# Kernel optimization log

Measured on AMD Instinct MI355X. Metric: run time of the kernel, lower is better.

## Reference

```python
import jax, jax.numpy as jnp
import numpy as np

N_NODES = 50000
N_EDGES = 800000
H = 128
LN_EPS = 1e-5


def setup_inputs() -> dict:
    key = jax.random.key(0)
    ks = jax.random.split(key, 8)
    x = jax.random.normal(ks[0], (N_NODES, H), dtype=jnp.float32)
    edge_index = jax.random.randint(ks[1], (2, N_EDGES), 0, N_NODES, dtype=jnp.int64)
    # edge_attention MLP params: Linear(2H -> H), ReLU, Linear(H -> 1), Sigmoid
    W1 = jax.random.normal(ks[2], (2 * H, H), dtype=jnp.float32) * 0.02
    b1 = jnp.zeros((H,), dtype=jnp.float32)
    W2 = jax.random.normal(ks[3], (H, 1), dtype=jnp.float32) * 0.02
    b2 = jnp.zeros((1,), dtype=jnp.float32)
    # LayerNorm affine params
    gamma = jnp.ones((H,), dtype=jnp.float32)
    beta = jnp.zeros((H,), dtype=jnp.float32)
    return {"x": x, "edge_index": edge_index, "W1": W1, "b1": b1,
            "W2": W2, "b2": b2, "gamma": gamma, "beta": beta}


def reference(x, edge_index, W1, b1, W2, b2, gamma, beta):
    src = edge_index[0]
    tgt = edge_index[1]
    # per-edge gated weight: sigmoid(MLP([x_src, x_tgt]))  -> [E]
    edge_feat = jnp.concatenate([x[src], x[tgt]], axis=1)        # [E, 2H]
    h = jax.nn.relu(edge_feat @ W1 + b1)                          # [E, H]
    w = jax.nn.sigmoid(h @ W2 + b2)[:, 0]                         # [E]
    # scatter-add weighted source features into targets (fused replacement
    # for the per-node Python loop in the original)
    agg = jax.ops.segment_sum(w[:, None] * x[src], tgt,
                              num_segments=x.shape[0])            # [N, H]
    attended = x + agg
    # LayerNorm over last dim
    mu = jnp.mean(attended, axis=-1, keepdims=True)
    var = jnp.mean(jnp.square(attended - mu), axis=-1, keepdims=True)
    out = (attended - mu) * jax.lax.rsqrt(var + LN_EPS) * gamma + beta
    return out
```

## Files before the change

kernel.cpp:

```cpp
#include <hip/hip_runtime.h>

static __device__ __forceinline__ unsigned short f2bf(float f) {
    union { float f; unsigned int u; } c; c.f = f;
    unsigned int u = c.u;
    return (unsigned short)((u + 0x7FFFu + ((u >> 16) & 1u)) >> 16);
}
static __device__ __forceinline__ float bflo(unsigned int uu) {
    union { unsigned int u; float f; } c; c.u = uu << 16; return c.f;
}
static __device__ __forceinline__ float bfhi(unsigned int uu) {
    union { unsigned int u; float f; } c; c.u = uu & 0xffff0000u; return c.f;
}
static __device__ __forceinline__ unsigned char f2fp8(float f) {
    int enc = __builtin_amdgcn_cvt_pk_fp8_f32(f, f, 0, false);
    return (unsigned char)(enc & 0xff);
}

typedef __bf16 bf16x8 __attribute__((ext_vector_type(8)));
typedef float  f32x4  __attribute__((ext_vector_type(4)));
typedef float  f32x2  __attribute__((ext_vector_type(2)));

__global__ void k_pack(const float* __restrict__ W1, unsigned short* __restrict__ Bt,
                       int* __restrict__ rowstart, int N) {
    int idx = blockIdx.x * blockDim.x + threadIdx.x;
    if (idx < 256 * 128) {
        int j = idx >> 7, k = idx & 127;
        int r = (j < 128) ? k : (128 + k);
        int c = j & 127;
        Bt[idx] = f2bf(W1[r * 128 + c]);
    }
    if (idx <= N) rowstart[idx] = 0;
}

__global__ __launch_bounds__(256) void k_gemm(const float* __restrict__ x,
                                              const unsigned short* __restrict__ Bt,
                                              const float* __restrict__ b1,
                                              unsigned char* __restrict__ U,
                                              unsigned short* __restrict__ V,
                                              unsigned short* __restrict__ XB, int M) {
    int wave = threadIdx.x >> 6, lane = threadIdx.x & 63;
    int row0 = blockIdx.x * 64 + wave * 16;
    int col0 = blockIdx.y * 64;
    int lr = lane & 15;
    int lk = (lane >> 4) << 3;

    f32x4 acc[4] = {};
    int arow = row0 + lr;
    bool in = (arow < M);
    const float* xr = x + (size_t)arow * 128;
    bool emit_xb = (blockIdx.y == 0);

#pragma unroll
    for (int kk = 0; kk < 4; ++kk) {
        int k = kk * 32 + lk;
        union { bf16x8 v; unsigned short u[8]; } ua;
        if (in) {
            float4 f0 = *(const float4*)(xr + k);
            float4 f1 = *(const float4*)(xr + k + 4);
            ua.u[0] = f2bf(f0.x); ua.u[1] = f2bf(f0.y);
            ua.u[2] = f2bf(f0.z); ua.u[3] = f2bf(f0.w);
            ua.u[4] = f2bf(f1.x); ua.u[5] = f2bf(f1.y);
            ua.u[6] = f2bf(f1.z); ua.u[7] = f2bf(f1.w);
        } else {
#pragma unroll
            for (int i = 0; i < 8; ++i) ua.u[i] = 0;
        }
        if (emit_xb && in) *(bf16x8*)(XB + (size_t)arow * 128 + k) = ua.v;
#pragma unroll
        for (int nf = 0; nf < 4; ++nf) {
            int col = col0 + nf * 16 + lr;
            bf16x8 b = *(const bf16x8*)(Bt + col * 128 + k);
            acc[nf] = __builtin_amdgcn_mfma_f32_16x16x32_bf16(ua.v, b, acc[nf], 0, 0, 0);
        }
    }
    int rb = row0 + ((lane >> 4) << 2);
    if (col0 < 128) {
#pragma unroll
        for (int nf = 0; nf < 4; ++nf) {
            int feat = col0 + nf * 16 + lr;
#pragma unroll
            for (int r = 0; r < 4; ++r) {
                int node = rb + r;
                if (node < M) U[(size_t)node * 128 + feat] = f2fp8(acc[nf][r]);
            }
        }
    } else {
#pragma unroll
        for (int nf = 0; nf < 4; ++nf) {
            int feat = col0 + nf * 16 + lr - 128;
            float bias = b1[feat];
#pragma unroll
            for (int r = 0; r < 4; ++r) {
                int node = rb + r;
                if (node < M) V[(size_t)node * 128 + feat] = f2bf(acc[nf][r] + bias);
            }
        }
    }
}

__global__ void k_hist(const int* __restrict__ ei, int* __restrict__ deg,
                       int* __restrict__ rank, int E) {
    int e = blockIdx.x * blockDim.x + threadIdx.x;
    if (e < E) rank[e] = atomicAdd(deg + ei[E + e], 1);
}

__global__ void k_scan1(int* __restrict__ a, int* __restrict__ bsum, int N) {
    __shared__ int s0[256], s1[256];
    int tid = threadIdx.x;
    int n = blockIdx.x * 256 + tid;
    int v = (n < N) ? a[n] : 0;
    s0[tid] = v;
    __syncthreads();
    int* cur = s0; int* nxt = s1;
#pragma unroll
    for (int off = 1; off < 256; off <<= 1) {
        int val = cur[tid];
        if (tid >= off) val += cur[tid - off];
        nxt[tid] = val;
        __syncthreads();
        int* t = cur; cur = nxt; nxt = t;
    }
    if (n < N) a[n] = cur[tid] - v;
    if (tid == 255) bsum[blockIdx.x] = cur[255];
}

__global__ void k_scan2(int* __restrict__ bsum, int nb) {
    __shared__ int s0[256], s1[256];
    int tid = threadIdx.x;
    int v = (tid < nb) ? bsum[tid] : 0;
    s0[tid] = v;
    __syncthreads();
    int* cur = s0; int* nxt = s1;
#pragma unroll
    for (int off = 1; off < 256; off <<= 1) {
        int val = cur[tid];
        if (tid >= off) val += cur[tid - off];
        nxt[tid] = val;
        __syncthreads();
        int* t = cur; cur = nxt; nxt = t;
    }
    if (tid < nb) bsum[tid] = cur[tid] - v;
}

__global__ void k_scan3(int* __restrict__ rowstart, const int* __restrict__ bsum,
                        int N, int E) {
    int n = blockIdx.x * 256 + threadIdx.x;
    if (n < N) rowstart[n] = rowstart[n] + bsum[n >> 8];
    if (n == 0) rowstart[N] = E;
}

__global__ void k_scatter(const int* __restrict__ ei, const int* __restrict__ rowstart,
                          const int* __restrict__ rank, int* __restrict__ esrc, int E) {
    int e = blockIdx.x * blockDim.x + threadIdx.x;
    if (e < E) {
        int s = ei[e];
        int t = ei[E + e];
        esrc[rowstart[t] + rank[e]] = s;
    }
}

template <int USE_XB>
__global__ __launch_bounds__(256) void k_fused(const float* __restrict__ x,
                                               const unsigned char* __restrict__ U,
                                               const unsigned short* __restrict__ V,
                                               const unsigned short* __restrict__ XB,
                                               const int* __restrict__ rowstart,
                                               const int* __restrict__ esrc,
                                               const float* __restrict__ W2,
                                               const float* __restrict__ b2,
                                               const float* __restrict__ gamma,
                                               const float* __restrict__ beta,
                                               float* __restrict__ out, int N) {
    int row = blockIdx.x * 4 + (threadIdx.x >> 6);
    if (row >= N) return;
    int lane = threadIdx.x & 63;
    int el = lane & 7;
    int q  = lane >> 3;

    float w2r[16];
#pragma unroll
    for (int i = 0; i < 16; ++i) w2r[i] = W2[16 * q + i];
    float b2s = b2[0];

    const unsigned short* vp = V + (size_t)row * 128 + 16 * q;
    uint4 va = *(const uint4*)vp;
    uint4 vb = *(const uint4*)(vp + 8);
    float vf[16];
    vf[0]  = bflo(va.x); vf[1]  = bfhi(va.x);
    vf[2]  = bflo(va.y); vf[3]  = bfhi(va.y);
    vf[4]  = bflo(va.z); vf[5]  = bfhi(va.z);
    vf[6]  = bflo(va.w); vf[7]  = bfhi(va.w);
    vf[8]  = bflo(vb.x); vf[9]  = bfhi(vb.x);
    vf[10] = bflo(vb.y); vf[11] = bfhi(vb.y);
    vf[12] = bflo(vb.z); vf[13] = bfhi(vb.z);
    vf[14] = bflo(vb.w); vf[15] = bfhi(vb.w);

    int st = rowstart[row];
    int en = rowstart[row + 1];

    float2 xx = *(const float2*)(x + (size_t)row * 128 + 2 * lane);
    float a0 = xx.x, a1 = xx.y;

    for (int g = st; g < en; g += 8) {
        int e = g + el;
        bool val = (e < en);
        int s = val ? esrc[e] : 0;

        uint4 ua = *(const uint4*)(U + (size_t)s * 128 + 16 * q);
        f32x2 d0 = __builtin_amdgcn_cvt_pk_f32_fp8(ua.x, false);
        f32x2 d1 = __builtin_amdgcn_cvt_pk_f32_fp8(ua.x, true);
        f32x2 d2 = __builtin_amdgcn_cvt_pk_f32_fp8(ua.y, false);
        f32x2 d3 = __builtin_amdgcn_cvt_pk_f32_fp8(ua.y, true);
        f32x2 d4 = __builtin_amdgcn_cvt_pk_f32_fp8(ua.z, false);
        f32x2 d5 = __builtin_amdgcn_cvt_pk_f32_fp8(ua.z, true);
        f32x2 d6 = __builtin_amdgcn_cvt_pk_f32_fp8(ua.w, false);
        f32x2 d7 = __builtin_amdgcn_cvt_pk_f32_fp8(ua.w, true);

        float p = 0.0f;
        p = fmaf(fmaxf(d0.x + vf[0],  0.f), w2r[0],  p);
        p = fmaf(fmaxf(d0.y + vf[1],  0.f), w2r[1],  p);
        p = fmaf(fmaxf(d1.x + vf[2],  0.f), w2r[2],  p);
        p = fmaf(fmaxf(d1.y + vf[3],  0.f), w2r[3],  p);
        p = fmaf(fmaxf(d2.x + vf[4],  0.f), w2r[4],  p);
        p = fmaf(fmaxf(d2.y + vf[5],  0.f), w2r[5],  p);
        p = fmaf(fmaxf(d3.x + vf[6],  0.f), w2r[6],  p);
        p = fmaf(fmaxf(d3.y + vf[7],  0.f), w2r[7],  p);
        p = fmaf(fmaxf(d4.x + vf[8],  0.f), w2r[8],  p);
        p = fmaf(fmaxf(d4.y + vf[9],  0.f), w2r[9],  p);
        p = fmaf(fmaxf(d5.x + vf[10], 0.f), w2r[10], p);
        p = fmaf(fmaxf(d5.y + vf[11], 0.f), w2r[11], p);
        p = fmaf(fmaxf(d6.x + vf[12], 0.f), w2r[12], p);
        p = fmaf(fmaxf(d6.y + vf[13], 0.f), w2r[13], p);
        p = fmaf(fmaxf(d7.x + vf[14], 0.f), w2r[14], p);
        p = fmaf(fmaxf(d7.y + vf[15], 0.f), w2r[15], p);

        p += __shfl_xor(p, 8);
        p += __shfl_xor(p, 16);
        p += __shfl_xor(p, 32);

        float w = val ? 1.0f / (1.0f + __expf(-(p + b2s))) : 0.0f;

#pragma unroll
        for (int j = 0; j < 8; ++j) {
            float wj = __shfl(w, j);
            int   sj = __shfl(s, j);
            if (USE_XB) {
                unsigned int xv = *(const unsigned int*)(XB + (size_t)sj * 128 + 2 * lane);
                a0 = fmaf(wj, bflo(xv), a0);
                a1 = fmaf(wj, bfhi(xv), a1);
            } else {
                float2 xf = *(const float2*)(x + (size_t)sj * 128 + 2 * lane);
                a0 = fmaf(wj, xf.x, a0);
                a1 = fmaf(wj, xf.y, a1);
            }
        }
    }

    float s = a0 + a1;
#pragma unroll
    for (int off = 32; off; off >>= 1) s += __shfl_xor(s, off);
    float mu = s * (1.0f / 128.0f);
    float d0v = a0 - mu, d1v = a1 - mu;
    float qq = d0v * d0v + d1v * d1v;
#pragma unroll
    for (int off = 32; off; off >>= 1) qq += __shfl_xor(qq, off);
    float rstd = rsqrtf(qq * (1.0f / 128.0f) + 1e-5f);
    float2 gg = *(const float2*)(gamma + 2 * lane);
    float2 bb = *(const float2*)(beta + 2 * lane);
    float2 o;
    o.x = d0v * rstd * gg.x + bb.x;
    o.y = d1v * rstd * gg.y + bb.y;
    *(float2*)(out + (size_t)row * 128 + 2 * lane) = o;
}

extern "C" void kernel_launch(void* const* d_in, const int* in_sizes, int n_in,
                              void* d_out, int out_size, void* d_ws, size_t ws_size,
                              hipStream_t stream) {
    const float* x     = (const float*)d_in[0];
    const int*   ei    = (const int*)d_in[1];
    const float* W1    = (const float*)d_in[2];
    const float* b1    = (const float*)d_in[3];
    const float* W2    = (const float*)d_in[4];
    const float* b2    = (const float*)d_in[5];
    const float* gamma = (const float*)d_in[6];
    const float* beta  = (const float*)d_in[7];
    float* out = (float*)d_out;

    const int N = in_sizes[0] / 128;
    const int E = in_sizes[1] / 2;
    const int NB = (N + 255) / 256;

    char* w = (char*)d_ws;
    size_t off = 0;
    auto alloc = [&](size_t bytes) {
        char* p = w + off;
        off = (off + bytes + 255) & ~(size_t)255;
        return p;
    };
    unsigned short* Bt       = (unsigned short*)alloc(256 * 128 * 2);
    unsigned char*  U        = (unsigned char*)alloc((size_t)N * 128);
    unsigned short* V        = (unsigned short*)alloc((size_t)N * 128 * 2);
    int*            rowstart = (int*)alloc((size_t)(N + 1) * 4);
    int*            bsum     = (int*)alloc(256 * 4);
    int*            rank     = (int*)alloc((size_t)E * 4);
    int*            esrc     = (int*)alloc((size_t)E * 4);
    size_t off_noxb = off;
    unsigned short* XB       = (unsigned short*)alloc((size_t)N * 128 * 2);
    bool use_xb = (off <= ws_size);
    if (!use_xb) { XB = nullptr; off = off_noxb; }

    int PB = (N + 256) / 256;
    if (PB < 128) PB = 128;
    k_pack<<<PB, 256, 0, stream>>>(W1, Bt, rowstart, N);

    dim3 ggrid((N + 63) / 64, 4);
    k_gemm<<<ggrid, 256, 0, stream>>>(x, Bt, b1, U, V, XB, N);

    k_hist<<<(E + 255) / 256, 256, 0, stream>>>(ei, rowstart, rank, E);

    k_scan1<<<NB, 256, 0, stream>>>(rowstart, bsum, N);
    k_scan2<<<1, 256, 0, stream>>>(bsum, NB);
    k_scan3<<<NB, 256, 0, stream>>>(rowstart, bsum, N, E);

    k_scatter<<<(E + 255) / 256, 256, 0, stream>>>(ei, rowstart, rank, esrc, E);

    if (use_xb)
        k_fused<1><<<(N + 3) / 4, 256, 0, stream>>>(x, U, V, XB, rowstart, esrc,
                                                    W2, b2, gamma, beta, out, N);
    else
        k_fused<0><<<(N + 3) / 4, 256, 0, stream>>>(x, U, V, XB, rowstart, esrc,
                                                    W2, b2, gamma, beta, out, N);
}
```

Baseline: 171.3 us.

## Fuse weight packing with degree histogram, widen GEMM tiles, read bf16 self features

Merges the W1 packing kernel with the edge-degree histogram kernel and replaces the rowstart zeroing with a memset, removing one launch. The GEMM now computes 128 output columns per block across a 2-wide grid instead of 64 columns across 4, so each block converts its x rows once for twice the MFMA work. The fused aggregation kernel reads the node's own features from the bf16 copy instead of fp32 x, halving that load at some precision cost in the residual. The wider tile raises register use per thread and may lower occupancy.

Result: slower. 177.5 us (+3.6%).

```diff
diff --git a/kernel.cpp b/kernel.cpp
--- a/kernel.cpp
+++ b/kernel.cpp
@@ -20,8 +20,9 @@
 typedef float  f32x4  __attribute__((ext_vector_type(4)));
 typedef float  f32x2  __attribute__((ext_vector_type(2)));
 
-__global__ void k_pack(const float* __restrict__ W1, unsigned short* __restrict__ Bt,
-                       int* __restrict__ rowstart, int N) {
+__global__ void k_packhist(const float* __restrict__ W1, unsigned short* __restrict__ Bt,
+                           const int* __restrict__ ei, int* __restrict__ deg,
+                           int* __restrict__ rank, int E) {
     int idx = blockIdx.x * blockDim.x + threadIdx.x;
     if (idx < 256 * 128) {
         int j = idx >> 7, k = idx & 127;
@@ -29,7 +30,9 @@
         int c = j & 127;
         Bt[idx] = f2bf(W1[r * 128 + c]);
     }
-    if (idx <= N) rowstart[idx] = 0;
+    int nthreads = gridDim.x * blockDim.x;
+    for (int e = idx; e < E; e += nthreads)
+        rank[e] = atomicAdd(deg + ei[E + e], 1);
 }
 
 __global__ __launch_bounds__(256) void k_gemm(const float* __restrict__ x,
@@ -40,15 +43,18 @@
                                               unsigned short* __restrict__ XB, int M) {
     int wave = threadIdx.x >> 6, lane = threadIdx.x & 63;
     int row0 = blockIdx.x * 64 + wave * 16;
-    int col0 = blockIdx.y * 64;
+    int col0 = blockIdx.y * 128;
     int lr = lane & 15;
     int lk = (lane >> 4) << 3;
 
-    f32x4 acc[4] = {};
+    f32x4 acc[8];
+#pragma unroll
+    for (int i = 0; i < 8; ++i) acc[i] = (f32x4){0.f, 0.f, 0.f, 0.f};
+
     int arow = row0 + lr;
     bool in = (arow < M);
     const float* xr = x + (size_t)arow * 128;
-    bool emit_xb = (blockIdx.y == 0);
+    bool emit_xb = (XB != nullptr) && (blockIdx.y == 0);
 
 #pragma unroll
     for (int kk = 0; kk < 4; ++kk) {
@@ -67,17 +73,17 @@
         }
         if (emit_xb && in) *(bf16x8*)(XB + (size_t)arow * 128 + k) = ua.v;
 #pragma unroll
-        for (int nf = 0; nf < 4; ++nf) {
+        for (int nf = 0; nf < 8; ++nf) {
             int col = col0 + nf * 16 + lr;
             bf16x8 b = *(const bf16x8*)(Bt + col * 128 + k);
             acc[nf] = __builtin_amdgcn_mfma_f32_16x16x32_bf16(ua.v, b, acc[nf], 0, 0, 0);
         }
     }
     int rb = row0 + ((lane >> 4) << 2);
-    if (col0 < 128) {
-#pragma unroll
-        for (int nf = 0; nf < 4; ++nf) {
-            int feat = col0 + nf * 16 + lr;
+    if (blockIdx.y == 0) {
+#pragma unroll
+        for (int nf = 0; nf < 8; ++nf) {
+            int feat = nf * 16 + lr;
 #pragma unroll
             for (int r = 0; r < 4; ++r) {
                 int node = rb + r;
@@ -86,8 +92,8 @@
         }
     } else {
 #pragma unroll
-        for (int nf = 0; nf < 4; ++nf) {
-            int feat = col0 + nf * 16 + lr - 128;
+        for (int nf = 0; nf < 8; ++nf) {
+            int feat = nf * 16 + lr;
             float bias = b1[feat];
 #pragma unroll
             for (int r = 0; r < 4; ++r) {
@@ -96,12 +102,6 @@
             }
         }
     }
-}
-
-__global__ void k_hist(const int* __restrict__ ei, int* __restrict__ deg,
-                       int* __restrict__ rank, int E) {
-    int e = blockIdx.x * blockDim.x + threadIdx.x;
-    if (e < E) rank[e] = atomicAdd(deg + ei[E + e], 1);
 }
 
 __global__ void k_scan1(int* __restrict__ a, int* __restrict__ bsum, int N) {
@@ -198,8 +198,14 @@
     int st = rowstart[row];
     int en = rowstart[row + 1];
 
-    float2 xx = *(const float2*)(x + (size_t)row * 128 + 2 * lane);
-    float a0 = xx.x, a1 = xx.y;
+    float a0, a1;
+    if (USE_XB) {
+        unsigned int xv = *(const unsigned int*)(XB + (size_t)row * 128 + 2 * lane);
+        a0 = bflo(xv); a1 = bfhi(xv);
+    } else {
+        float2 xx = *(const float2*)(x + (size_t)row * 128 + 2 * lane);
+        a0 = xx.x; a1 = xx.y;
+    }
 
     for (int g = st; g < en; g += 8) {
         int e = g + el;
@@ -309,14 +315,12 @@
     bool use_xb = (off <= ws_size);
     if (!use_xb) { XB = nullptr; off = off_noxb; }
 
-    int PB = (N + 256) / 256;
-    if (PB < 128) PB = 128;
-    k_pack<<<PB, 256, 0, stream>>>(W1, Bt, rowstart, N);
-
-    dim3 ggrid((N + 63) / 64, 4);
+    hipMemsetAsync(rowstart, 0, (size_t)(N + 1) * 4, stream);
+
+    k_packhist<<<(E + 255) / 256, 256, 0, stream>>>(W1, Bt, ei, rowstart, rank, E);
+
+    dim3 ggrid((N + 63) / 64, 2);
     k_gemm<<<ggrid, 256, 0, stream>>>(x, Bt, b1, U, V, XB, N);
-
-    k_hist<<<(E + 255) / 256, 256, 0, stream>>>(ei, rowstart, rank, E);
 
     k_scan1<<<NB, 256, 0, stream>>>(rowstart, bsum, N);
     k_scan2<<<1, 256, 0, stream>>>(bsum, NB);
```

## Unroll edge loop by two, merge scan passes, read self row from bf16

Applied to the files above, without the earlier changes.

The fused aggregation loop now handles 16 edges per iteration as two independent groups of 8. This doubles the gathers and shuffles in flight to hide the latency of the random loads. The second and third scan kernels are merged into one, where each block rescans the block sums itself, removing one launch. The node's own row is now read from the bf16 copy, which slightly changes precision for the residual term, and the gemm skips writing XB when it is null.

New measurement: 174.5 us. No clear change (+1.9%).

```diff
diff --git a/kernel.cpp b/kernel.cpp
--- a/kernel.cpp
+++ b/kernel.cpp
@@ -19,6 +19,36 @@
 typedef __bf16 bf16x8 __attribute__((ext_vector_type(8)));
 typedef float  f32x4  __attribute__((ext_vector_type(4)));
 typedef float  f32x2  __attribute__((ext_vector_type(2)));
+
+static __device__ __forceinline__ float mlp16(uint4 ua, const float* __restrict__ vf,
+                                              const float* __restrict__ w2r) {
+    f32x2 d0 = __builtin_amdgcn_cvt_pk_f32_fp8(ua.x, false);
+    f32x2 d1 = __builtin_amdgcn_cvt_pk_f32_fp8(ua.x, true);
+    f32x2 d2 = __builtin_amdgcn_cvt_pk_f32_fp8(ua.y, false);
+    f32x2 d3 = __builtin_amdgcn_cvt_pk_f32_fp8(ua.y, true);
+    f32x2 d4 = __builtin_amdgcn_cvt_pk_f32_fp8(ua.z, false);
+    f32x2 d5 = __builtin_amdgcn_cvt_pk_f32_fp8(ua.z, true);
+    f32x2 d6 = __builtin_amdgcn_cvt_pk_f32_fp8(ua.w, false);
+    f32x2 d7 = __builtin_amdgcn_cvt_pk_f32_fp8(ua.w, true);
+    float p = 0.0f;
+    p = fmaf(fmaxf(d0.x + vf[0],  0.f), w2r[0],  p);
+    p = fmaf(fmaxf(d0.y + vf[1],  0.f), w2r[1],  p);
+    p = fmaf(fmaxf(d1.x + vf[2],  0.f), w2r[2],  p);
+    p = fmaf(fmaxf(d1.y + vf[3],  0.f), w2r[3],  p);
+    p = fmaf(fmaxf(d2.x + vf[4],  0.f), w2r[4],  p);
+    p = fmaf(fmaxf(d2.y + vf[5],  0.f), w2r[5],  p);
+    p = fmaf(fmaxf(d3.x + vf[6],  0.f), w2r[6],  p);
+    p = fmaf(fmaxf(d3.y + vf[7],  0.f), w2r[7],  p);
+    p = fmaf(fmaxf(d4.x + vf[8],  0.f), w2r[8],  p);
+    p = fmaf(fmaxf(d4.y + vf[9],  0.f), w2r[9],  p);
+    p = fmaf(fmaxf(d5.x + vf[10], 0.f), w2r[10], p);
+    p = fmaf(fmaxf(d5.y + vf[11], 0.f), w2r[11], p);
+    p = fmaf(fmaxf(d6.x + vf[12], 0.f), w2r[12], p);
+    p = fmaf(fmaxf(d6.y + vf[13], 0.f), w2r[13], p);
+    p = fmaf(fmaxf(d7.x + vf[14], 0.f), w2r[14], p);
+    p = fmaf(fmaxf(d7.y + vf[15], 0.f), w2r[15], p);
+    return p;
+}
 
 __global__ void k_pack(const float* __restrict__ W1, unsigned short* __restrict__ Bt,
                        int* __restrict__ rowstart, int N) {
@@ -48,7 +78,7 @@
     int arow = row0 + lr;
     bool in = (arow < M);
     const float* xr = x + (size_t)arow * 128;
-    bool emit_xb = (blockIdx.y == 0);
+    bool emit_xb = (XB != nullptr) && (blockIdx.y == 0);
 
 #pragma unroll
     for (int kk = 0; kk < 4; ++kk) {
@@ -124,11 +154,11 @@
     if (tid == 255) bsum[blockIdx.x] = cur[255];
 }
 
-__global__ void k_scan2(int* __restrict__ bsum, int nb) {
+__global__ void k_scan23(int* __restrict__ rowstart, const int* __restrict__ bsum,
+                         int nb, int N, int E) {
     __shared__ int s0[256], s1[256];
     int tid = threadIdx.x;
-    int v = (tid < nb) ? bsum[tid] : 0;
-    s0[tid] = v;
+    s0[tid] = (tid < nb) ? bsum[tid] : 0;
     __syncthreads();
     int* cur = s0; int* nxt = s1;
 #pragma unroll
@@ -139,13 +169,10 @@
         __syncthreads();
         int* t = cur; cur = nxt; nxt = t;
     }
-    if (tid < nb) bsum[tid] = cur[tid] - v;
-}
-
-__global__ void k_scan3(int* __restrict__ rowstart, const int* __restrict__ bsum,
-                        int N, int E) {
-    int n = blockIdx.x * 256 + threadIdx.x;
-    if (n < N) rowstart[n] = rowstart[n] + bsum[n >> 8];
+    int b = blockIdx.x;
+    int offset = (b == 0) ? 0 : cur[b - 1];
+    int n = b * 256 + tid;
+    if (n < N) rowstart[n] += offset;
     if (n == 0) rowstart[N] = E;
 }
 
@@ -198,60 +225,56 @@
     int st = rowstart[row];
     int en = rowstart[row + 1];
 
-    float2 xx = *(const float2*)(x + (size_t)row * 128 + 2 * lane);
-    float a0 = xx.x, a1 = xx.y;
-
-    for (int g = st; g < en; g += 8) {
-        int e = g + el;
-        bool val = (e < en);
-        int s = val ? esrc[e] : 0;
-
-        uint4 ua = *(const uint4*)(U + (size_t)s * 128 + 16 * q);
-        f32x2 d0 = __builtin_amdgcn_cvt_pk_f32_fp8(ua.x, false);
-        f32x2 d1 = __builtin_amdgcn_cvt_pk_f32_fp8(ua.x, true);
-        f32x2 d2 = __builtin_amdgcn_cvt_pk_f32_fp8(ua.y, false);
-        f32x2 d3 = __builtin_amdgcn_cvt_pk_f32_fp8(ua.y, true);
-        f32x2 d4 = __builtin_amdgcn_cvt_pk_f32_fp8(ua.z, false);
-        f32x2 d5 = __builtin_amdgcn_cvt_pk_f32_fp8(ua.z, true);
-        f32x2 d6 = __builtin_amdgcn_cvt_pk_f32_fp8(ua.w, false);
-        f32x2 d7 = __builtin_amdgcn_cvt_pk_f32_fp8(ua.w, true);
-
-        float p = 0.0f;
-        p = fmaf(fmaxf(d0.x + vf[0],  0.f), w2r[0],  p);
-        p = fmaf(fmaxf(d0.y + vf[1],  0.f), w2r[1],  p);
-        p = fmaf(fmaxf(d1.x + vf[2],  0.f), w2r[2],  p);
-        p = fmaf(fmaxf(d1.y + vf[3],  0.f), w2r[3],  p);
-        p = fmaf(fmaxf(d2.x + vf[4],  0.f), w2r[4],  p);
-        p = fmaf(fmaxf(d2.y + vf[5],  0.f), w2r[5],  p);
-        p = fmaf(fmaxf(d3.x + vf[6],  0.f), w2r[6],  p);
-        p = fmaf(fmaxf(d3.y + vf[7],  0.f), w2r[7],  p);
-        p = fmaf(fmaxf(d4.x + vf[8],  0.f), w2r[8],  p);
-        p = fmaf(fmaxf(d4.y + vf[9],  0.f), w2r[9],  p);
-        p = fmaf(fmaxf(d5.x + vf[10], 0.f), w2r[10], p);
-        p = fmaf(fmaxf(d5.y + vf[11], 0.f), w2r[11], p);
-        p = fmaf(fmaxf(d6.x + vf[12], 0.f), w2r[12], p);
-        p = fmaf(fmaxf(d6.y + vf[13], 0.f), w2r[13], p);
-        p = fmaf(fmaxf(d7.x + vf[14], 0.f), w2r[14], p);
-        p = fmaf(fmaxf(d7.y + vf[15], 0.f), w2r[15], p);
-
-        p += __shfl_xor(p, 8);
-        p += __shfl_xor(p, 16);
-        p += __shfl_xor(p, 32);
-
-        float w = val ? 1.0f / (1.0f + __expf(-(p + b2s))) : 0.0f;
+    float a0, a1;
+    if (USE_XB) {
+        unsigned int xv = *(const unsigned int*)(XB + (size_t)row * 128 + 2 * lane);
+        a0 = bflo(xv); a1 = bfhi(xv);
+    } else {
+        float2 xx = *(const float2*)(x + (size_t)row * 128 + 2 * lane);
+        a0 = xx.x; a1 = xx.y;
+    }
+
+    for (int g = st; g < en; g += 16) {
+        int e0 = g + el;
+        int e1 = g + 8 + el;
+        bool v0 = (e0 < en);
+        bool v1 = (e1 < en);
+        int s0 = v0 ? esrc[e0] : 0;
+        int s1 = v1 ? esrc[e1] : 0;
+
+        uint4 ua0 = *(const uint4*)(U + (size_t)s0 * 128 + 16 * q);
+        uint4 ua1 = *(const uint4*)(U + (size_t)s1 * 128 + 16 * q);
+
+        float p0 = mlp16(ua0, vf, w2r);
+        float p1 = mlp16(ua1, vf, w2r);
+
+        p0 += __shfl_xor(p0, 8);  p1 += __shfl_xor(p1, 8);
+        p0 += __shfl_xor(p0, 16); p1 += __shfl_xor(p1, 16);
+        p0 += __shfl_xor(p0, 32); p1 += __shfl_xor(p1, 32);
+
+        float w0 = v0 ? 1.0f / (1.0f + __expf(-(p0 + b2s))) : 0.0f;
+        float w1 = v1 ? 1.0f / (1.0f + __expf(-(p1 + b2s))) : 0.0f;
 
 #pragma unroll
         for (int j = 0; j < 8; ++j) {
-            float wj = __shfl(w, j);
-            int   sj = __shfl(s, j);
+            int   sj0 = __shfl(s0, j);
+            int   sj1 = __shfl(s1, j);
+            float wj0 = __shfl(w0, j);
+            float wj1 = __shfl(w1, j);
             if (USE_XB) {
-                unsigned int xv = *(const unsigned int*)(XB + (size_t)sj * 128 + 2 * lane);
-                a0 = fmaf(wj, bflo(xv), a0);
-                a1 = fmaf(wj, bfhi(xv), a1);
+                unsigned int xv0 = *(const unsigned int*)(XB + (size_t)sj0 * 128 + 2 * lane);
+                unsigned int xv1 = *(const unsigned int*)(XB + (size_t)sj1 * 128 + 2 * lane);
+                a0 = fmaf(wj0, bflo(xv0), a0);
+                a1 = fmaf(wj0, bfhi(xv0), a1);
+                a0 = fmaf(wj1, bflo(xv1), a0);
+                a1 = fmaf(wj1, bfhi(xv1), a1);
             } else {
-                float2 xf = *(const float2*)(x + (size_t)sj * 128 + 2 * lane);
-                a0 = fmaf(wj, xf.x, a0);
-                a1 = fmaf(wj, xf.y, a1);
+                float2 xf0 = *(const float2*)(x + (size_t)sj0 * 128 + 2 * lane);
+                float2 xf1 = *(const float2*)(x + (size_t)sj1 * 128 + 2 * lane);
+                a0 = fmaf(wj0, xf0.x, a0);
+                a1 = fmaf(wj0, xf0.y, a1);
+                a0 = fmaf(wj1, xf1.x, a0);
+                a1 = fmaf(wj1, xf1.y, a1);
             }
         }
     }
@@ -319,8 +342,7 @@
     k_hist<<<(E + 255) / 256, 256, 0, stream>>>(ei, rowstart, rank, E);
 
     k_scan1<<<NB, 256, 0, stream>>>(rowstart, bsum, N);
-    k_scan2<<<1, 256, 0, stream>>>(bsum, NB);
-    k_scan3<<<NB, 256, 0, stream>>>(rowstart, bsum, N, E);
+    k_scan23<<<NB, 256, 0, stream>>>(rowstart, bsum, NB, N, E);
 
     k_scatter<<<(E + 255) / 256, 256, 0, stream>>>(ei, rowstart, rank, esrc, E);
 
```

## Fuse prep kernels, merge scan passes, and read bf16 x everywhere

Applied to the files above, without the earlier changes.

Weight packing, the x-to-bf16 conversion and the degree histogram are merged into one grid-stride prep kernel, and the rowstart zeroing moves to a memset. The GEMM now reads the precomputed bf16 XB instead of converting fp32 x itself. Scan passes 2 and 3 are merged, with each block redundantly scanning the block sums. The fused kernel now takes the residual x from bf16 XB, which lowers precision, and the fp32 fallback for a small workspace is removed.

Result: no change. 171.2 us (-0.0%).

```diff
diff --git a/kernel.cpp b/kernel.cpp
--- a/kernel.cpp
+++ b/kernel.cpp
@@ -20,24 +20,35 @@
 typedef float  f32x4  __attribute__((ext_vector_type(4)));
 typedef float  f32x2  __attribute__((ext_vector_type(2)));
 
-__global__ void k_pack(const float* __restrict__ W1, unsigned short* __restrict__ Bt,
-                       int* __restrict__ rowstart, int N) {
+__global__ void k_prep(const float* __restrict__ W1, unsigned short* __restrict__ Bt,
+                       const float* __restrict__ x, unsigned short* __restrict__ XB,
+                       const int* __restrict__ ei, int* __restrict__ deg,
+                       int* __restrict__ rank, int NH4 , int E) {
     int idx = blockIdx.x * blockDim.x + threadIdx.x;
+    int T = gridDim.x * blockDim.x;
+
     if (idx < 256 * 128) {
         int j = idx >> 7, k = idx & 127;
         int r = (j < 128) ? k : (128 + k);
-        int c = j & 127;
-        Bt[idx] = f2bf(W1[r * 128 + c]);
-    }
-    if (idx <= N) rowstart[idx] = 0;
-}
-
-__global__ __launch_bounds__(256) void k_gemm(const float* __restrict__ x,
+        Bt[idx] = f2bf(W1[r * 128 + (j & 127)]);
+    }
+
+    for (int i = idx; i < NH4; i += T) {
+        float4 f = ((const float4*)x)[i];
+        ushort4 o;
+        o.x = f2bf(f.x); o.y = f2bf(f.y); o.z = f2bf(f.z); o.w = f2bf(f.w);
+        ((ushort4*)XB)[i] = o;
+    }
+
+    for (int e = idx; e < E; e += T)
+        rank[e] = atomicAdd(deg + ei[E + e], 1);
+}
+
+__global__ __launch_bounds__(256) void k_gemm(const unsigned short* __restrict__ XB,
                                               const unsigned short* __restrict__ Bt,
                                               const float* __restrict__ b1,
                                               unsigned char* __restrict__ U,
-                                              unsigned short* __restrict__ V,
-                                              unsigned short* __restrict__ XB, int M) {
+                                              unsigned short* __restrict__ V, int M) {
     int wave = threadIdx.x >> 6, lane = threadIdx.x & 63;
     int row0 = blockIdx.x * 64 + wave * 16;
     int col0 = blockIdx.y * 64;
@@ -47,30 +58,18 @@
     f32x4 acc[4] = {};
     int arow = row0 + lr;
     bool in = (arow < M);
-    const float* xr = x + (size_t)arow * 128;
-    bool emit_xb = (blockIdx.y == 0);
+    const unsigned short* xr = XB + (size_t)arow * 128;
 
 #pragma unroll
     for (int kk = 0; kk < 4; ++kk) {
         int k = kk * 32 + lk;
-        union { bf16x8 v; unsigned short u[8]; } ua;
-        if (in) {
-            float4 f0 = *(const float4*)(xr + k);
-            float4 f1 = *(const float4*)(xr + k + 4);
-            ua.u[0] = f2bf(f0.x); ua.u[1] = f2bf(f0.y);
-            ua.u[2] = f2bf(f0.z); ua.u[3] = f2bf(f0.w);
-            ua.u[4] = f2bf(f1.x); ua.u[5] = f2bf(f1.y);
-            ua.u[6] = f2bf(f1.z); ua.u[7] = f2bf(f1.w);
-        } else {
-#pragma unroll
-            for (int i = 0; i < 8; ++i) ua.u[i] = 0;
-        }
-        if (emit_xb && in) *(bf16x8*)(XB + (size_t)arow * 128 + k) = ua.v;
+        bf16x8 a = {};
+        if (in) a = *(const bf16x8*)(xr + k);
 #pragma unroll
         for (int nf = 0; nf < 4; ++nf) {
             int col = col0 + nf * 16 + lr;
             bf16x8 b = *(const bf16x8*)(Bt + col * 128 + k);
-            acc[nf] = __builtin_amdgcn_mfma_f32_16x16x32_bf16(ua.v, b, acc[nf], 0, 0, 0);
+            acc[nf] = __builtin_amdgcn_mfma_f32_16x16x32_bf16(a, b, acc[nf], 0, 0, 0);
         }
     }
     int rb = row0 + ((lane >> 4) << 2);
@@ -96,12 +95,6 @@
             }
         }
     }
-}
-
-__global__ void k_hist(const int* __restrict__ ei, int* __restrict__ deg,
-                       int* __restrict__ rank, int E) {
-    int e = blockIdx.x * blockDim.x + threadIdx.x;
-    if (e < E) rank[e] = atomicAdd(deg + ei[E + e], 1);
 }
 
 __global__ void k_scan1(int* __restrict__ a, int* __restrict__ bsum, int N) {
@@ -124,11 +117,11 @@
     if (tid == 255) bsum[blockIdx.x] = cur[255];
 }
 
-__global__ void k_scan2(int* __restrict__ bsum, int nb) {
+__global__ void k_scan23(int* __restrict__ rowstart, const int* __restrict__ bsum,
+                         int nb, int N, int E) {
     __shared__ int s0[256], s1[256];
     int tid = threadIdx.x;
-    int v = (tid < nb) ? bsum[tid] : 0;
-    s0[tid] = v;
+    s0[tid] = (tid < nb) ? bsum[tid] : 0;
     __syncthreads();
     int* cur = s0; int* nxt = s1;
 #pragma unroll
@@ -139,13 +132,10 @@
         __syncthreads();
         int* t = cur; cur = nxt; nxt = t;
     }
-    if (tid < nb) bsum[tid] = cur[tid] - v;
-}
-
-__global__ void k_scan3(int* __restrict__ rowstart, const int* __restrict__ bsum,
-                        int N, int E) {
-    int n = blockIdx.x * 256 + threadIdx.x;
-    if (n < N) rowstart[n] = rowstart[n] + bsum[n >> 8];
+    int b = blockIdx.x;
+    int offset = (b == 0) ? 0 : cur[b - 1];
+    int n = b * 256 + tid;
+    if (n < N) rowstart[n] += offset;
     if (n == 0) rowstart[N] = E;
 }
 
@@ -159,9 +149,7 @@
     }
 }
 
-template <int USE_XB>
-__global__ __launch_bounds__(256) void k_fused(const float* __restrict__ x,
-                                               const unsigned char* __restrict__ U,
+__global__ __launch_bounds__(256) void k_fused(const unsigned char* __restrict__ U,
                                                const unsigned short* __restrict__ V,
                                                const unsigned short* __restrict__ XB,
                                                const int* __restrict__ rowstart,
@@ -198,8 +186,8 @@
     int st = rowstart[row];
     int en = rowstart[row + 1];
 
-    float2 xx = *(const float2*)(x + (size_t)row * 128 + 2 * lane);
-    float a0 = xx.x, a1 = xx.y;
+    unsigned int xvr = *(const unsigned int*)(XB + (size_t)row * 128 + 2 * lane);
+    float a0 = bflo(xvr), a1 = bfhi(xvr);
 
     for (int g = st; g < en; g += 8) {
         int e = g + el;
@@ -244,15 +232,9 @@
         for (int j = 0; j < 8; ++j) {
             float wj = __shfl(w, j);
             int   sj = __shfl(s, j);
-            if (USE_XB) {
-                unsigned int xv = *(const unsigned int*)(XB + (size_t)sj * 128 + 2 * lane);
-                a0 = fmaf(wj, bflo(xv), a0);
-                a1 = fmaf(wj, bfhi(xv), a1);
-            } else {
-                float2 xf = *(const float2*)(x + (size_t)sj * 128 + 2 * lane);
-                a0 = fmaf(wj, xf.x, a0);
-                a1 = fmaf(wj, xf.y, a1);
-            }
+            unsigned int xv = *(const unsigned int*)(XB + (size_t)sj * 128 + 2 * lane);
+            a0 = fmaf(wj, bflo(xv), a0);
+            a1 = fmaf(wj, bfhi(xv), a1);
         }
     }
 
@@ -304,30 +286,21 @@
     int*            bsum     = (int*)alloc(256 * 4);
     int*            rank     = (int*)alloc((size_t)E * 4);
     int*            esrc     = (int*)alloc((size_t)E * 4);
-    size_t off_noxb = off;
     unsigned short* XB       = (unsigned short*)alloc((size_t)N * 128 * 2);
-    bool use_xb = (off <= ws_size);
-    if (!use_xb) { XB = nullptr; off = off_noxb; }
-
-    int PB = (N + 256) / 256;
-    if (PB < 128) PB = 128;
-    k_pack<<<PB, 256, 0, stream>>>(W1, Bt, rowstart, N);
+
+    hipMemsetAsync(rowstart, 0, (size_t)(N + 1) * 4, stream);
+
+    k_prep<<<(E + 255) / 256, 256, 0, stream>>>(W1, Bt, x, XB, ei, rowstart,
+                                                rank, N * 128 / 4, E);
 
     dim3 ggrid((N + 63) / 64, 4);
-    k_gemm<<<ggrid, 256, 0, stream>>>(x, Bt, b1, U, V, XB, N);
-
-    k_hist<<<(E + 255) / 256, 256, 0, stream>>>(ei, rowstart, rank, E);
+    k_gemm<<<ggrid, 256, 0, stream>>>(XB, Bt, b1, U, V, N);
 
     k_scan1<<<NB, 256, 0, stream>>>(rowstart, bsum, N);
-    k_scan2<<<1, 256, 0, stream>>>(bsum, NB);
-    k_scan3<<<NB, 256, 0, stream>>>(rowstart, bsum, N, E);
+    k_scan23<<<NB, 256, 0, stream>>>(rowstart, bsum, NB, N, E);
 
     k_scatter<<<(E + 255) / 256, 256, 0, stream>>>(ei, rowstart, rank, esrc, E);
 
-    if (use_xb)
-        k_fused<1><<<(N + 3) / 4, 256, 0, stream>>>(x, U, V, XB, rowstart, esrc,
-                                                    W2, b2, gamma, beta, out, N);
-    else
-        k_fused<0><<<(N + 3) / 4, 256, 0, stream>>>(x, U, V, XB, rowstart, esrc,
-                                                    W2, b2, gamma, beta, out, N);
-}
+    k_fused<<<(N + 3) / 4, 256, 0, stream>>>(U, V, XB, rowstart, esrc,
+                                             W2, b2, gamma, beta, out, N);
+}
```
